# Kernel tuning notes

Measured on AMD Instinct MI355X. Metric: run time of the kernel, lower is better.

## Reference

```python
import jax, jax.numpy as jnp
import numpy as np

N = 20000      # nodes
E = 1280000    # edges
F = 42         # num_features (forced equal to mpnn out_channels by the code)
H = 20         # lstm hidden per direction


def setup_inputs() -> dict:
    key = jax.random.key(0)
    ks = jax.random.split(key, 17)
    def rn(k, shape, sc=0.1):
        return jax.random.normal(k, shape, dtype=jnp.float32) * sc
    return {
        "x": rn(ks[0], (N, F), 1.0),
        "edge_index": jax.random.randint(ks[1], (2, E), 0, N),
        "edge_attr": jax.random.uniform(ks[2], (E, 1), dtype=jnp.float32),
        "lin_w": rn(ks[3], (F, 2 * F)),
        "lin_b": rn(ks[4], (F,)),
        "gru_w_ih": rn(ks[5], (3 * F, F)),
        "gru_w_hh": rn(ks[6], (3 * F, F)),
        "gru_b_ih": rn(ks[7], (3 * F,)),
        "gru_b_hh": rn(ks[8], (3 * F,)),
        "lstm_w_ih_f": rn(ks[9], (4 * H, F)),
        "lstm_w_hh_f": rn(ks[10], (4 * H, H)),
        "lstm_b_f": rn(ks[11], (4 * H,)),
        "lstm_w_ih_b": rn(ks[12], (4 * H, F)),
        "lstm_w_hh_b": rn(ks[13], (4 * H, H)),
        "lstm_b_b": rn(ks[14], (4 * H,)),
        "cls_w": rn(ks[15], (1, 2 * H)),
        "cls_b": rn(ks[16], (1,)),
    }


def _lstm_dir(xs, w_ih, w_hh, b):
    # xs: [N, F] treated as a length-N sequence with batch 1
    x_proj = xs @ w_ih.T + b  # [N, 4H] precompute input contribution
    def cell(carry, xp):
        h, c = carry
        g = xp + w_hh @ h                      # [4H]
        i, f, gg, o = jnp.split(g, 4)
        c = jax.nn.sigmoid(f) * c + jax.nn.sigmoid(i) * jnp.tanh(gg)
        h = jax.nn.sigmoid(o) * jnp.tanh(c)
        return (h, c), h
    h0 = jnp.zeros((H,), xs.dtype)
    _, hs = jax.lax.scan(cell, (h0, h0), x_proj)
    return hs  # [N, H]


def reference(x, edge_index, edge_attr, lin_w, lin_b,
              gru_w_ih, gru_w_hh, gru_b_ih, gru_b_hh,
              lstm_w_ih_f, lstm_w_hh_f, lstm_b_f,
              lstm_w_ih_b, lstm_w_hh_b, lstm_b_b,
              cls_w, cls_b):
    n = x.shape[0]
    src, dst = edge_index[0], edge_index[1]
    # --- message: gather x_i (target) / x_j (source), concat-linear, sigmoid gate
    x_i = x[dst]                               # [E, F]
    x_j = x[src]                               # [E, F]
    msg = jnp.concatenate([x_i, x_j], axis=1) @ lin_w.T + lin_b  # [E, F]
    msg = msg * jax.nn.sigmoid(-edge_attr)     # gate on -time_diff, broadcast [E,1]
    # --- aggregate: scatter-add at target nodes
    agg = jax.ops.segment_sum(msg, dst, num_segments=n)  # [N, F]
    # --- GRU, seq_len=1, batch=N, input = hidden init = agg
    gi = agg @ gru_w_ih.T + gru_b_ih           # [N, 3F]
    gh = agg @ gru_w_hh.T + gru_b_hh           # [N, 3F]
    i_r, i_z, i_n = jnp.split(gi, 3, axis=1)
    h_r, h_z, h_n = jnp.split(gh, 3, axis=1)
    r = jax.nn.sigmoid(i_r + h_r)
    z = jax.nn.sigmoid(i_z + h_z)
    ng = jnp.tanh(i_n + r * h_n)
    hx = (1.0 - z) * ng + z * agg              # [N, F]
    # --- bidirectional LSTM over nodes as a sequence (batch=1)
    h_fwd = _lstm_dir(hx, lstm_w_ih_f, lstm_w_hh_f, lstm_b_f)                # [N, H]
    h_bwd = _lstm_dir(hx[::-1], lstm_w_ih_b, lstm_w_hh_b, lstm_b_b)[::-1]    # [N, H]
    h_cat = jnp.concatenate([h_fwd, h_bwd], axis=1)  # [N, 2H]
    return h_cat @ cls_w.T + cls_b             # [N, 1]
```

## Files before the change

### kernel.cpp

```cpp
#include <hip/hip_runtime.h>

#define NN 20000
#define EE 1280000
#define FF 42
#define HH 20
#define PSTR 44

#define CHUNK 25
#define WARM 50
#define NCH 800
#define TT 16

#define NBIN 625
#define BINW 32
#define CAP  2560
#define NCHKB 160
#define CHKE 8000
#define NSC (NBIN*NCHKB)
#define NSB1 ((NSC+255)/256)

__device__ __forceinline__ float fexp2(float x){ return __builtin_amdgcn_exp2f(x); }
__device__ __forceinline__ float frcp(float x){ return __builtin_amdgcn_rcpf(x); }
__device__ __forceinline__ float fsigmoid(float x){ return frcp(1.f + fexp2(-1.442695041f*x)); }
__device__ __forceinline__ float ftanh(float x){ return 2.f*frcp(1.f + fexp2(-2.885390082f*x)) - 1.f; }

__global__ __launch_bounds__(256) void k_nodeproj(
    const float* __restrict__ x, const float* __restrict__ lw,
    float* __restrict__ PA, float* __restrict__ PB)
{
  __shared__ float2 w1S[FF*21];
  __shared__ float2 w2S[FF*21];
  for (int idx=threadIdx.x; idx<FF*21; idx+=256){
    int k = idx/21, fp = idx - 21*k;
    w1S[idx] = make_float2(lw[(2*fp)*84 + k],      lw[(2*fp+1)*84 + k]);
    w2S[idx] = make_float2(lw[(2*fp)*84 + 42 + k], lw[(2*fp+1)*84 + 42 + k]);
  }
  __syncthreads();
  int tid = blockIdx.x*256 + threadIdx.x;
  if (tid >= NN*21) return;
  int n = tid / 21;
  int fp = tid - n*21;
  const float* xr = x + n*FF;
  float2 pa = make_float2(0.f,0.f), pb = make_float2(0.f,0.f);
#pragma unroll 6
  for (int k=0;k<FF;k++){
    float xv = xr[k];
    float2 w1 = w1S[k*21+fp], w2 = w2S[k*21+fp];
    pa.x += w1.x*xv; pa.y += w1.y*xv;
    pb.x += w2.x*xv; pb.y += w2.y*xv;
  }
  ((float2*)(PA + n*PSTR))[fp] = pa;
  ((float2*)(PB + n*PSTR))[fp] = pb;
  if (fp == 0){
    PA[n*PSTR+42] = 0.f; PA[n*PSTR+43] = 0.f;
    PB[n*PSTR+42] = 0.f; PB[n*PSTR+43] = 0.f;
  }
}

__global__ __launch_bounds__(256) void k_binA(const int* __restrict__ dst, int* __restrict__ cnt)
{
  __shared__ unsigned int h[NBIN];
  int blk = blockIdx.x, tid = threadIdx.x;
  for (int i=tid; i<NBIN; i+=256) h[i] = 0;
  __syncthreads();
  const int* d = dst + blk*CHKE;
  for (int i=tid; i<CHKE; i+=256) atomicAdd(&h[d[i]>>5], 1u);
  __syncthreads();
  for (int i=tid; i<NBIN; i+=256) cnt[i*NCHKB + blk] = (int)h[i];
}

__global__ __launch_bounds__(256) void k_scan1(int* __restrict__ cnt, int* __restrict__ bsum)
{
  int b = blockIdx.x, t = threadIdx.x;
  int i = b*256 + t;
  int v = (i < NSC) ? cnt[i] : 0;
  int lane = t & 63, w = t >> 6;
  int x = v;
#pragma unroll
  for (int off=1; off<64; off<<=1){
    int y = __shfl_up(x, off);
    if (lane >= off) x += y;
  }
  __shared__ int wsum[4];
  if (lane == 63) wsum[w] = x;
  __syncthreads();
  int base = 0;
  for (int ww=0; ww<w; ww++) base += wsum[ww];
  int incl = x + base;
  if (i < NSC) cnt[i] = incl - v;
  if (t == 255) bsum[b] = incl;
}

__global__ __launch_bounds__(1024) void k_scan2(const int* __restrict__ bsum, int* __restrict__ boff)
{
  int t = threadIdx.x;
  int v = (t < NSB1) ? bsum[t] : 0;
  int lane = t & 63, w = t >> 6;
  int x = v;
#pragma unroll
  for (int off=1; off<64; off<<=1){
    int y = __shfl_up(x, off);
    if (lane >= off) x += y;
  }
  __shared__ int ws2[16];
  if (lane == 63) ws2[w] = x;
  __syncthreads();
  int base = 0;
  for (int ww=0; ww<w; ww++) base += ws2[ww];
  int incl = x + base;
  if (t < NSB1) boff[t] = incl - v;
}

__global__ __launch_bounds__(256) void k_binC(
    const int* __restrict__ src, const int* __restrict__ dst,
    const float* __restrict__ ea, const int* __restrict__ cnt,
    const int* __restrict__ boff, int2* __restrict__ binned)
{
  __shared__ unsigned int cur[NBIN];
  int blk = blockIdx.x, tid = threadIdx.x;
  for (int i=tid; i<NBIN; i+=256){
    int idx = i*NCHKB + blk;
    cur[i] = (unsigned)(cnt[idx] + boff[idx>>8]);
  }
  __syncthreads();
  for (int i=tid; i<CHKE; i+=256){
    int e = blk*CHKE + i;
    int d = dst[e];
    int s = src[e];
    float g = fsigmoid(-ea[e]);
    unsigned p = atomicAdd(&cur[d>>5], 1u);
    int2 r; r.x = s | ((d & 31) << 16); r.y = __float_as_int(g);
    binned[p] = r;
  }
}

__global__ __launch_bounds__(512, 8) void k_agg(
    const float* __restrict__ PA, const float* __restrict__ PB,
    const int* __restrict__ cnt, const int* __restrict__ boff,
    const int2* __restrict__ binned, const float* __restrict__ lin_b,
    float* __restrict__ agg)
{
  __shared__ int2 edS[CAP];
  __shared__ unsigned int cntL[BINW];
  __shared__ unsigned int offsN[BINW+1];
  __shared__ float lbS[PSTR];

  int b = blockIdx.x, tid = threadIdx.x;
  if (tid < PSTR) lbS[tid] = (tid < FF) ? lin_b[tid] : 0.f;
  int i0g = b*NCHKB;
  int e0 = cnt[i0g] + boff[i0g>>8];
  int e1;
  if (b == NBIN-1) e1 = EE;
  else { int i1g = (b+1)*NCHKB; e1 = cnt[i1g] + boff[i1g>>8]; }
  int cl = e1 - e0; if (cl > CAP) cl = CAP;

  int2 E[5];
  if (tid < BINW) cntL[tid] = 0;
  __syncthreads();
#pragma unroll
  for (int u=0; u<5; u++){
    int i = tid + u*512;
    if (i < cl){
      E[u] = binned[e0+i];
      atomicAdd(&cntL[E[u].x >> 16], 1u);
    }
  }
  __syncthreads();
  if (tid < 64){
    unsigned v = (tid < BINW) ? cntL[tid] : 0u;
    unsigned x = v;
#pragma unroll
    for (int off=1; off<32; off<<=1){
      unsigned y = __shfl_up(x, off);
      if ((tid & 63) >= off) x += y;
    }
    if (tid < BINW) offsN[tid+1] = x;
    if (tid == 0) offsN[0] = 0;
  }
  __syncthreads();
  if (tid < BINW) cntL[tid] = offsN[tid];
  __syncthreads();
#pragma unroll
  for (int u=0; u<5; u++){
    int i = tid + u*512;
    if (i < cl){
      unsigned p = atomicAdd(&cntL[E[u].x >> 16], 1u);
      edS[p] = E[u];
    }
  }
  __syncthreads();

  int w = tid >> 6, lane = tid & 63;
  int grp = lane / 11;
  int fp  = lane - grp*11;
  bool lact = grp < 5;
  unsigned a0[4], aE[4];
  int M = 0;
#pragma unroll
  for (int j=0;j<4;j++){
    int n = w + 8*j;
    a0[j] = offsN[n]; aE[j] = offsN[n+1];
    int len = (int)(aE[j]-a0[j]); if (len > M) M = len;
  }
  float4 acc[4]; float gs[4];
#pragma unroll
  for (int j=0;j<4;j++){ acc[j]=make_float4(0.f,0.f,0.f,0.f); gs[j]=0.f; }
  for (int t=0; t<M; t+=5){
    float4 pv[4]; float gv[4];
#pragma unroll
    for (int j=0;j<4;j++){
      unsigned k = a0[j] + (unsigned)(t + grp);
      bool v = lact && (k < aE[j]);
      unsigned ks = v ? k : 0u;
      int2 Ee = edS[ks];
      gv[j] = v ? __int_as_float(Ee.y) : 0.f;
      pv[j] = ((const float4*)(PB + (Ee.x & 0xFFFF)*PSTR))[fp];
    }
#pragma unroll
    for (int j=0;j<4;j++){
      acc[j].x += gv[j]*pv[j].x;  acc[j].y += gv[j]*pv[j].y;
      acc[j].z += gv[j]*pv[j].z;  acc[j].w += gv[j]*pv[j].w;
      gs[j]    += gv[j];
    }
  }
#pragma unroll
  for (int j=0;j<4;j++){
    float vx=acc[j].x, vy=acc[j].y, vz=acc[j].z, vw=acc[j].w, g=gs[j];
#pragma unroll
    for (int s=1;s<5;s++){
      vx += __shfl(acc[j].x, lane + 11*s);
      vy += __shfl(acc[j].y, lane + 11*s);
      vz += __shfl(acc[j].z, lane + 11*s);
      vw += __shfl(acc[j].w, lane + 11*s);
      g  += __shfl(gs[j],    lane + 11*s);
    }
    if (lane < 11){
      int n = w + 8*j;
      const float4 pa = ((const float4*)(PA + (b*BINW+n)*PSTR))[fp];
      float4 lb = ((const float4*)lbS)[fp];
      float4 o;
      o.x = (pa.x + lb.x)*g + vx;
      o.y = (pa.y + lb.y)*g + vy;
      o.z = (pa.z + lb.z)*g + vz;
      o.w = (pa.w + lb.w)*g + vw;
      ((float4*)(agg + (b*BINW+n)*PSTR))[fp] = o;
    }
  }
}

#define GNOD 64
#define GSTR 45
__global__ __launch_bounds__(1024, 4) void k_gru(
    const float* __restrict__ agg,
    const float* __restrict__ gwih, const float* __restrict__ gwhh,
    const float* __restrict__ gbih, const float* __restrict__ gbhh,
    const float* __restrict__ lwihf, const float* __restrict__ lbf,
    const float* __restrict__ lwihb, const float* __restrict__ lbb,
    float* __restrict__ xpf, float* __restrict__ xpb)
{
  __shared__ float aggL[GNOD*GSTR];
  __shared__ float hxL [GNOD*GSTR];
  int b = blockIdx.x, tid = threadIdx.x;
  int node = tid & 63;
  int n = b*GNOD + node;
  int slot = __builtin_amdgcn_readfirstlane(tid >> 6);

  for (int idx=tid; idx<GNOD*11; idx+=1024){
    int nd = idx/11, c = idx - 11*nd;
    int gn = b*GNOD + nd;
    if (gn < NN){
      float4 v = ((const float4*)(agg + gn*PSTR))[c];
      float* d = aggL + nd*GSTR + 4*c;
      d[0]=v.x; d[1]=v.y; d[2]=v.z; d[3]=v.w;
    }
  }
  __syncthreads();

  bool act = n < NN;
  const float* Arow = aggL + node*GSTR;

#pragma unroll 1
  for (int jj=0; jj<3; jj++){
    int j = slot + 16*jj;
    if (j < FF){
      float ir = gbih[j], iz = gbih[FF+j], inn = gbih[2*FF+j];
      float hr = gbhh[j], hz = gbhh[FF+j], hn  = gbhh[2*FF+j];
      const float* Wi0 = gwih + j*FF;
      const float* Wi1 = gwih + (FF+j)*FF;
      const float* Wi2 = gwih + (2*FF+j)*FF;
      const float* Wh0 = gwhh + j*FF;
      const float* Wh1 = gwhh + (FF+j)*FF;
      const float* Wh2 = gwhh + (2*FF+j)*FF;
#pragma unroll
      for (int k=0;k<FF;k++){
        float a = Arow[k];
        ir += Wi0[k]*a;  iz += Wi1[k]*a;  inn += Wi2[k]*a;
        hr += Wh0[k]*a;  hz += Wh1[k]*a;  hn  += Wh2[k]*a;
      }
      float r  = fsigmoid(ir+hr);
      float z  = fsigmoid(iz+hz);
      float ng = ftanh(inn + r*hn);
      hxL[node*GSTR + j] = (1.f - z)*ng + z*Arow[j];
    }
  }
  __syncthreads();

  const float* Hrow = hxL + node*GSTR;

#pragma unroll 1
  for (int ro=0; ro<10; ro++){
    int gq = slot + 16*ro;
    bool fw = gq < 80;
    int g = fw ? gq : gq - 80;
    const float* Wp = (fw ? lwihf : lwihb) + g*FF;
    float d = fw ? lbf[g] : lbb[g];
#pragma unroll
    for (int k=0;k<FF;k++) d += Wp[k]*Hrow[k];
    if (act){
      float* dstp = fw ? xpf : xpb;
      dstp[n*80 + g] = d;
    }
  }
}

__global__ __launch_bounds__(64) void k_lstm(
    const float* __restrict__ xpf, const float* __restrict__ xpb,
    const float* __restrict__ whhf, const float* __restrict__ whhb,
    float* __restrict__ hf, float* __restrict__ hb)
{
  __shared__ float buf[2][TT*80];
  int b = blockIdx.x;
  int dir = b / NCH;
  int chunk = b - dir*NCH;
  const float* xp  = dir ? xpb  : xpf;
  const float* whh = dir ? whhb : whhf;
  float* hout      = dir ? hb   : hf;

  int lane = threadIdx.x;
  int m = lane & 31;
  int half = lane >> 5;
  int mm = (m < HH) ? m : HH-1;
  int rowA = half*40 + mm;
  int rowB = rowA + HH;
  float2 WA[10], WB[10];
#pragma unroll
  for (int kk=0;kk<10;kk++){
    WA[kk] = make_float2(whh[rowA*HH+2*kk], whh[rowA*HH+2*kk+1]);
    WB[kk] = make_float2(whh[rowB*HH+2*kk], whh[rowB*HH+2*kk+1]);
  }
  const float cE = half ? -2.885390082f : -1.442695041f;
  const float cM = half ? 2.f : 1.f;
  const float cA = half ? -1.f : 0.f;
  int colA = rowA;
  int colB = rowB;

  int p0 = chunk*CHUNK;
  int ps = (p0 >= WARM) ? (p0-WARM) : 0;
  int p1 = p0 + CHUNK;
  int steps = p1 - ps;
  int ntiles = (steps + TT - 1)/TT;

  float4 R0,R1,R2,R3,R4;
  auto fetch = [&](int j){
    int a = ps + j*TT;
    long g0;
    if (!dir) g0 = (long)a*80;
    else { int t_lo = NN - a - TT; if (t_lo < 0) t_lo = 0; g0 = (long)t_lo*80; }
    const float* s = xp + g0 + lane*4;
    R0 = *(const float4*)(s);
    R1 = *(const float4*)(s + 256);
    R2 = *(const float4*)(s + 512);
    R3 = *(const float4*)(s + 768);
    R4 = *(const float4*)(s + 1024);
  };
  auto stash = [&](int dbuf){
    float* d = buf[dbuf] + lane*4;
    *(float4*)(d)        = R0;
    *(float4*)(d + 256)  = R1;
    *(float4*)(d + 512)  = R2;
    *(float4*)(d + 768)  = R3;
    *(float4*)(d + 1024) = R4;
  };

  fetch(0); stash(0);
  if (ntiles > 1) fetch(1);

  float c = 0.f, h = 0.f;
  float2 H[10];
#pragma unroll
  for (int kk=0;kk<10;kk++) H[kk] = make_float2(0.f, 0.f);

  int t_lo0 = 0;
  if (dir){ t_lo0 = NN - ps - TT; if (t_lo0 < 0) t_lo0 = 0; }
  int row0 = dir ? (NN-1-ps - t_lo0) : 0;
  float nxA = buf[0][row0*80 + colA];
  float nxB = buf[0][row0*80 + colB];

  for (int j=0; j<ntiles; ++j){
    if (j+1 < ntiles) stash((j+1)&1);
    if (j+2 < ntiles) fetch(j+2);
    const float* B  = buf[j&1];
    const float* Bn = buf[(j+1)&1];
    int a = ps + j*TT;
    int t_lo = 0;
    if (dir){ t_lo = NN - a - TT; if (t_lo < 0) t_lo = 0; }
    int aN = a + TT;
    int t_loN = 0;
    if (dir){ t_loN = NN - aN - TT; if (t_loN < 0) t_loN = 0; }
#pragma unroll 4
    for (int r=0; r<TT; ++r){
      int p = a + r;
      float xA = nxA, xB = nxB;
      if (r+1 < TT){
        int rowN = dir ? (NN-1-(p+1) - t_lo) : (r+1);
        nxA = B[rowN*80 + colA];
        nxB = B[rowN*80 + colB];
      } else if (j+1 < ntiles){
        int rowN = dir ? (NN-1-aN - t_loN) : 0;
        nxA = Bn[rowN*80 + colA];
        nxB = Bn[rowN*80 + colB];
      }
      float aA0=xA, aA1=0.f, aB0=xB, aB1=0.f;
#pragma unroll
      for (int kk=0;kk<10;kk++){
        aA0 += WA[kk].x*H[kk].x;  aA1 += WA[kk].y*H[kk].y;
        aB0 += WB[kk].x*H[kk].x;  aB1 += WB[kk].y*H[kk].y;
      }
      float gA = aA0+aA1, gB = aB0+aB1;
      float actA = cM*frcp(1.f + fexp2(cE*gA)) + cA;
      float actB = frcp(1.f + fexp2(-1.442695041f*gB));
      float gT = __shfl_xor(actA, 32);
      float oT = __shfl_xor(actB, 32);
      c = actB*c + actA*gT;
      h = oT*ftanh(c);
#pragma unroll
      for (int kk=0;kk<10;kk++){
        float va = __int_as_float(__builtin_amdgcn_readlane(__float_as_int(h), 2*kk));
        float vb = __int_as_float(__builtin_amdgcn_readlane(__float_as_int(h), 2*kk+1));
        H[kk] = make_float2(va, vb);
      }
      if (p >= p0 && p < p1 && lane < HH){
        int t = dir ? (NN-1-p) : p;
        hout[t*HH + lane] = h;
      }
    }
  }
}

__global__ __launch_bounds__(256) void k_cls(
    const float* __restrict__ hf, const float* __restrict__ hb,
    const float* __restrict__ cw, const float* __restrict__ cb,
    float* __restrict__ out)
{
  int n = blockIdx.x*256 + threadIdx.x;
  if (n >= NN) return;
  float s = cb[0];
  const float* hfr = hf + n*HH;
  const float* hbr = hb + n*HH;
#pragma unroll
  for (int k=0;k<HH;k++){
    s += hfr[k]*cw[k] + hbr[k]*cw[HH+k];
  }
  out[n] = s;
}

extern "C" void kernel_launch(void* const* d_in, const int* in_sizes, int n_in,
                              void* d_out, int out_size, void* d_ws, size_t ws_size,
                              hipStream_t stream) {
  (void)in_sizes; (void)n_in; (void)out_size; (void)ws_size;
  const float* x      = (const float*)d_in[0];
  const int*   ei     = (const int*)  d_in[1];
  const float* ea     = (const float*)d_in[2];
  const float* lin_w  = (const float*)d_in[3];
  const float* lin_b  = (const float*)d_in[4];
  const float* gwih   = (const float*)d_in[5];
  const float* gwhh   = (const float*)d_in[6];
  const float* gbih   = (const float*)d_in[7];
  const float* gbhh   = (const float*)d_in[8];
  const float* lwihf  = (const float*)d_in[9];
  const float* lwhhf  = (const float*)d_in[10];
  const float* lbf    = (const float*)d_in[11];
  const float* lwihb  = (const float*)d_in[12];
  const float* lwhhb  = (const float*)d_in[13];
  const float* lbb    = (const float*)d_in[14];
  const float* cw     = (const float*)d_in[15];
  const float* cb     = (const float*)d_in[16];
  float* out = (float*)d_out;

  const int* src = ei;
  const int* dst = ei + EE;

  float* PA     = (float*)d_ws;
  float* PB     = PA + NN*PSTR;
  float* agg    = PB + NN*PSTR;
  float* xpf    = agg + NN*PSTR;
  float* xpb    = xpf + NN*80;
  float* hf     = xpb + NN*80;
  float* hb     = hf + NN*HH;
  int2*  binned = (int2*)(hb + NN*HH);
  int*   cnt    = (int*)(binned + EE);
  int*   bsum   = cnt + NSC;
  int*   boff   = bsum + NSB1;

  k_nodeproj<<<(NN*21 + 255)/256, 256, 0, stream>>>(x, lin_w, PA, PB);
  k_binA<<<NCHKB, 256, 0, stream>>>(dst, cnt);
  k_scan1<<<NSB1, 256, 0, stream>>>(cnt, bsum);
  k_scan2<<<1, 1024, 0, stream>>>(bsum, boff);
  k_binC<<<NCHKB, 256, 0, stream>>>(src, dst, ea, cnt, boff, binned);
  k_agg<<<NBIN, 512, 0, stream>>>(PA, PB, cnt, boff, binned, lin_b, agg);
  k_gru<<<(NN + GNOD - 1)/GNOD, 1024, 0, stream>>>(agg, gwih, gwhh, gbih, gbhh,
                                                   lwihf, lbf, lwihb, lbb, xpf, xpb);
  k_lstm<<<2*NCH, 64, 0, stream>>>(xpf, xpb, lwhhf, lwhhb, hf, hb);
  k_cls<<<(NN + 255)/256, 256, 0, stream>>>(hf, hb, cw, cb, out);
}
```

Baseline: 248.1 us.

## Halve LSTM chunk length and pack four chunk-waves per block

The chunked LSTM recurrence now uses chunks of 12 steps instead of 25, giving 1667 chunks per direction. Four independent chunk wavefronts are packed into each 256-thread block, each with its own shared-memory double buffer. Shorter chunks shorten the serial critical path, but the fixed 50-step warmup becomes a larger share of each chunk's work. Bounds checks were added for the final partial chunk.

```diff
diff --git a/kernel.cpp b/kernel.cpp
--- a/kernel.cpp
+++ b/kernel.cpp
@@ -6,9 +6,11 @@
 #define HH 20
 #define PSTR 44
 
-#define CHUNK 25
+#define CHUNK 12
 #define WARM 50
-#define NCH 800
+#define NCHD 1667
+#define TOTCH (2*NCHD)
+#define LW 4
 #define TT 16
 
 #define NBIN 625
@@ -323,20 +325,27 @@
   }
 }
 
-__global__ __launch_bounds__(64) void k_lstm(
+__global__ __launch_bounds__(256) void k_lstm(
     const float* __restrict__ xpf, const float* __restrict__ xpb,
     const float* __restrict__ whhf, const float* __restrict__ whhb,
     float* __restrict__ hf, float* __restrict__ hb)
 {
-  __shared__ float buf[2][TT*80];
-  int b = blockIdx.x;
-  int dir = b / NCH;
-  int chunk = b - dir*NCH;
+  __shared__ float bufAll[LW][2][TT*80];
+  int wv = threadIdx.x >> 6;
+  int lane = threadIdx.x & 63;
+  int c = blockIdx.x*LW + wv;
+  if (c >= TOTCH) return;
+  int dir = (c >= NCHD) ? 1 : 0;
+  int chunk = c - dir*NCHD;
+  int p0 = chunk*CHUNK;
+  if (p0 >= NN) return;
+  int p1 = p0 + CHUNK; if (p1 > NN) p1 = NN;
+
   const float* xp  = dir ? xpb  : xpf;
   const float* whh = dir ? whhb : whhf;
   float* hout      = dir ? hb   : hf;
-
-  int lane = threadIdx.x;
+  float (*buf)[TT*80] = bufAll[wv];
+
   int m = lane & 31;
   int half = lane >> 5;
   int mm = (m < HH) ? m : HH-1;
@@ -354,9 +363,7 @@
   int colA = rowA;
   int colB = rowB;
 
-  int p0 = chunk*CHUNK;
   int ps = (p0 >= WARM) ? (p0-WARM) : 0;
-  int p1 = p0 + CHUNK;
   int steps = p1 - ps;
   int ntiles = (steps + TT - 1)/TT;
 
@@ -385,7 +392,7 @@
   fetch(0); stash(0);
   if (ntiles > 1) fetch(1);
 
-  float c = 0.f, h = 0.f;
+  float c2 = 0.f, h = 0.f;
   float2 H[10];
 #pragma unroll
   for (int kk=0;kk<10;kk++) H[kk] = make_float2(0.f, 0.f);
@@ -413,8 +420,10 @@
       float xA = nxA, xB = nxB;
       if (r+1 < TT){
         int rowN = dir ? (NN-1-(p+1) - t_lo) : (r+1);
-        nxA = B[rowN*80 + colA];
-        nxB = B[rowN*80 + colB];
+        if (p+1 < ps+steps || !dir){
+          nxA = B[rowN*80 + colA];
+          nxB = B[rowN*80 + colB];
+        }
       } else if (j+1 < ntiles){
         int rowN = dir ? (NN-1-aN - t_loN) : 0;
         nxA = Bn[rowN*80 + colA];
@@ -431,8 +440,8 @@
       float actB = frcp(1.f + fexp2(-1.442695041f*gB));
       float gT = __shfl_xor(actA, 32);
       float oT = __shfl_xor(actB, 32);
-      c = actB*c + actA*gT;
-      h = oT*ftanh(c);
+      c2 = actB*c2 + actA*gT;
+      h = oT*ftanh(c2);
 #pragma unroll
       for (int kk=0;kk<10;kk++){
         float va = __int_as_float(__builtin_amdgcn_readlane(__float_as_int(h), 2*kk));
@@ -510,6 +519,6 @@
   k_agg<<<NBIN, 512, 0, stream>>>(PA, PB, cnt, boff, binned, lin_b, agg);
   k_gru<<<(NN + GNOD - 1)/GNOD, 1024, 0, stream>>>(agg, gwih, gwhh, gbih, gbhh,
                                                    lwihf, lbf, lwihb, lbb, xpf, xpb);
-  k_lstm<<<2*NCH, 64, 0, stream>>>(xpf, xpb, lwhhf, lwhhb, hf, hb);
+  k_lstm<<<(TOTCH + LW - 1)/LW, 256, 0, stream>>>(xpf, xpb, lwhhf, lwhhb, hf, hb);
   k_cls<<<(NN + 255)/256, 256, 0, stream>>>(hf, hb, cw, cb, out);
 }
```

After: 261.4 us. 5.3% more time.
